# Performance work log

Hardware: AMD Instinct MI355X
Metric: run time of the kernel (lower is better)

## Reference

```python
import jax, jax.numpy as jnp
import numpy as np

NUM_HEADS = 16
ROPE_BASE = 10000.0


def _rope_cos_sin(seq_len, head_dim, dtype):
    # freqs for the half-dim; original caches cat(freqs, freqs) and then applies
    # the rotation per-half, which is equivalent to using the half-size tables.
    inv_freq = 1.0 / (ROPE_BASE ** (jnp.arange(0, head_dim, 2, dtype=jnp.float32) / head_dim))
    t = jnp.arange(seq_len, dtype=jnp.float32)
    freqs = jnp.einsum('i,j->ij', t, inv_freq)  # [S, hd/2]
    return jnp.cos(freqs).astype(dtype), jnp.sin(freqs).astype(dtype)


def _apply_rotary(x, cos, sin):
    # x: [B, H, S, hd]; cos/sin: [S, hd/2] broadcast over B, H
    half = x.shape[-1] // 2
    x1, x2 = x[..., :half], x[..., half:]
    return jnp.concatenate([x1 * cos - x2 * sin, x2 * cos + x1 * sin], axis=-1)


def setup_inputs() -> dict:
    key = jax.random.key(0)
    ks = jax.random.split(key, 5)
    D = 2048
    B, S = 2, 2048
    std = 1.0 / np.sqrt(D)
    return {
        'x': jax.random.normal(ks[0], (B, S, D), dtype=jnp.float32),
        'Wq': jax.random.normal(ks[1], (D, D), dtype=jnp.float32) * std,
        'Wk': jax.random.normal(ks[2], (D, D), dtype=jnp.float32) * std,
        'Wv': jax.random.normal(ks[3], (D, D), dtype=jnp.float32) * std,
        'Wo': jax.random.normal(ks[4], (D, D), dtype=jnp.float32) * std,
    }


def reference(x, Wq, Wk, Wv, Wo):
    B, S, D = x.shape
    H = NUM_HEADS
    hd = D // H
    scale = hd ** -0.5

    def proj(W):  # torch Linear: y = x @ W.T -> [B, H, S, hd]
        return (x @ W.T).reshape(B, S, H, hd).transpose(0, 2, 1, 3)

    q, k, v = proj(Wq), proj(Wk), proj(Wv)

    cos, sin = _rope_cos_sin(S, hd, x.dtype)
    q = _apply_rotary(q, cos, sin)
    k = _apply_rotary(k, cos, sin)

    scores = jnp.einsum('bhqd,bhkd->bhqk', q, k) * scale  # full O(S^2) scores
    attn = jax.nn.softmax(scores, axis=-1)
    out = jnp.einsum('bhqk,bhkd->bhqd', attn, v)
    out = out.transpose(0, 2, 1, 3).reshape(B, S, D)
    return out @ Wo.T
```

## Files before the change

kernel.cpp:

```cpp
#include <hip/hip_runtime.h>
#include <cstdint>

typedef __attribute__((ext_vector_type(8))) short bf16x8;
typedef __attribute__((ext_vector_type(4))) float f32x4;
typedef __attribute__((ext_vector_type(16))) float f32x16;

__device__ inline unsigned short f2bf(float f) {
  uint32_t u = __float_as_uint(f);
  uint32_t lsb = (u >> 16) & 1u;
  u += 0x7fffu + lsb;
  return (unsigned short)(u >> 16);
}
__device__ inline float bf2f(unsigned short b) {
  return __uint_as_float(((uint32_t)b) << 16);
}
__device__ inline uint32_t cvt_pk_bf16(float lo, float hi) {
  uint32_t r;
  asm volatile("v_cvt_pk_bf16_f32 %0, %1, %2" : "=v"(r) : "v"(lo), "v"(hi));
  return r;
}

#define GLOAD16(gp, lp)                                                        \
  __builtin_amdgcn_global_load_lds(                                            \
      (const __attribute__((address_space(1))) void*)(gp),                     \
      (__attribute__((address_space(3))) void*)(lp), 16, 0, 0)

__global__ void cvt_f32_bf16(const float* __restrict__ in,
                             unsigned short* __restrict__ out, int n) {
  int i = (blockIdx.x * 256 + threadIdx.x) * 4;
  if (i >= n) return;
  float4 v = *(const float4*)(in + i);
  unsigned short o[4] = {f2bf(v.x), f2bf(v.y), f2bf(v.z), f2bf(v.w)};
  *(uint64_t*)(out + i) = *(const uint64_t*)o;
}

__global__ void rope_table_k(float* __restrict__ ctab, float* __restrict__ stab) {
  int i = blockIdx.x * 256 + threadIdx.x;
  int s = i >> 6, j = i & 63;
  float invf = expf(-(float)j * (9.210340371976184f / 64.0f));
  float ang = (float)s * invf;
  ctab[i] = cosf(ang);
  stab[i] = sinf(ang);
}

__global__ void rope_apply_k(unsigned short* __restrict__ qb,
                             unsigned short* __restrict__ kb,
                             const float* __restrict__ ctab,
                             const float* __restrict__ stab) {
  int row = blockIdx.x * 4 + (threadIdx.x >> 6);
  int t = threadIdx.x & 63;
  int s = row & 2047;
  int bh = (row >> 11) & 31;
  int isK = row >> 16;
  unsigned short* base = isK ? kb : qb;
  float qs = isK ? 1.0f : (0.08838834764831845f * 1.4426950408889634f);
  unsigned short* p = base + ((size_t)bh * 2048 + s) * 128;
  float c = ctab[s * 64 + t], sn = stab[s * 64 + t];
  float x1 = bf2f(p[t]), x2 = bf2f(p[t + 64]);
  p[t] = f2bf((x1 * c - x2 * sn) * qs);
  p[t + 64] = f2bf((x2 * c + x1 * sn) * qs);
}

__global__ void transpose_v_k(const unsigned short* __restrict__ v,
                              unsigned short* __restrict__ vt) {
  __shared__ unsigned short tile[64][72];
  int bh = blockIdx.x, st = blockIdx.y, dt = blockIdx.z;
  const unsigned short* src = v + ((size_t)bh * 2048 + st * 64) * 128 + dt * 64;
  unsigned short* dst = vt + ((size_t)bh * 128 + dt * 64) * 2048 + st * 64;
  int t = threadIdx.x;
  int r = t >> 2, c0 = (t & 3) * 16;
  *(bf16x8*)&tile[r][c0] = *(const bf16x8*)(src + (size_t)r * 128 + c0);
  *(bf16x8*)&tile[r][c0 + 8] = *(const bf16x8*)(src + (size_t)r * 128 + c0 + 8);
  __syncthreads();
  unsigned short o[16];
#pragma unroll
  for (int i = 0; i < 16; i++) o[i] = tile[c0 + i][r];
  *(bf16x8*)(dst + (size_t)r * 2048 + c0) = *(const bf16x8*)&o[0];
  *(bf16x8*)(dst + (size_t)r * 2048 + c0 + 8) = *(const bf16x8*)&o[8];
}

template <int EPI>
__global__ __launch_bounds__(256, 2) void gemm_bt(
    const unsigned short* __restrict__ A, const unsigned short* __restrict__ Bm,
    float* __restrict__ Cf, unsigned short* __restrict__ q_out,
    unsigned short* __restrict__ k_out, unsigned short* __restrict__ v_out,
    int M, int N, int K) {
  __shared__ unsigned short sA[128 * 32];
  __shared__ unsigned short sB[128 * 32];
  const int t = threadIdx.x;
  const int w = t >> 6, l = t & 63;
  const int wr = w >> 1, wc = w & 1;
  const int bm = blockIdx.x * 128, bn = blockIdx.y * 128;
  const int lr = l & 15, lg = l >> 4;
  f32x4 acc[4][4] = {};

  const int srow = w * 16 + (l >> 2);
  const int sseg = (l & 3) * 8;
  const unsigned short* ga = A + (size_t)(bm + srow) * K + sseg;
  const unsigned short* gb = Bm + (size_t)(bn + srow) * K + sseg;
  unsigned short* lA = sA + w * 512 + l * 8;
  unsigned short* lB = sB + w * 512 + l * 8;

  for (int kt = 0; kt < K; kt += 32) {
    __syncthreads();
    GLOAD16(ga + kt, lA);
    GLOAD16(ga + kt + (size_t)64 * K, lA + 2048);
    GLOAD16(gb + kt, lB);
    GLOAD16(gb + kt + (size_t)64 * K, lB + 2048);
    __syncthreads();
    bf16x8 af[4], bfv[4];
#pragma unroll
    for (int m = 0; m < 4; m++)
      af[m] = *(const bf16x8*)(sA + (wr * 64 + m * 16 + lr) * 32 + lg * 8);
#pragma unroll
    for (int n = 0; n < 4; n++)
      bfv[n] = *(const bf16x8*)(sB + (wc * 64 + n * 16 + lr) * 32 + lg * 8);
#pragma unroll
    for (int m = 0; m < 4; m++)
#pragma unroll
      for (int n = 0; n < 4; n++)
        acc[m][n] = __builtin_amdgcn_mfma_f32_16x16x32_bf16(af[m], bfv[n],
                                                            acc[m][n], 0, 0, 0);
  }

#pragma unroll
  for (int m = 0; m < 4; m++) {
#pragma unroll
    for (int n = 0; n < 4; n++) {
      int gm0 = bm + wr * 64 + m * 16 + lg * 4;
      int gn = bn + wc * 64 + n * 16 + lr;
#pragma unroll
      for (int j = 0; j < 4; j++) {
        float v = acc[m][n][j];
        int gm = gm0 + j;
        if (EPI == 0) {
          Cf[(size_t)gm * N + gn] = v;
        } else {
          int which = gn >> 11, rem = gn & 2047;
          int h = rem >> 7, d = rem & 127;
          int b = gm >> 11, s = gm & 2047;
          unsigned short* dst = which == 0 ? q_out : (which == 1 ? k_out : v_out);
          dst[(((size_t)(b * 16 + h)) * 2048 + s) * 128 + d] = f2bf(v);
        }
      }
    }
  }
}

__global__ __launch_bounds__(256, 2) void attn_k(
    const unsigned short* __restrict__ Q, const unsigned short* __restrict__ K,
    const unsigned short* __restrict__ Vt, unsigned short* __restrict__ ctx) {
  __shared__ unsigned short sK[2][64 * 128];
  __shared__ unsigned short sV[2][128 * 64];

  const int qt = blockIdx.x, bh = blockIdx.y;
  const int t = threadIdx.x;
  const int w = t >> 6, l = t & 63;
  const int lq = l & 31;
  const int h5 = l >> 5;
  const int b = bh >> 4, hh = bh & 15;
  const int q0 = qt * 128 + w * 32;
  const unsigned short* Qp = Q + ((size_t)bh * 2048 + q0) * 128;
  const unsigned short* Kbh = K + (size_t)bh * 2048 * 128;
  const unsigned short* Vbh = Vt + (size_t)bh * 128 * 2048;

  int gko[4], gvo[4];
#pragma unroll
  for (int i = 0; i < 4; i++) {
    int p = i * 256 + t;
    int rK = p >> 4, cK = p & 15;
    gko[i] = rK * 128 + ((cK ^ (rK & 7)) * 8);
    int rV = p >> 3, cV = p & 7;
    gvo[i] = rV * 2048 + ((cV ^ (rV & 7)) * 8);
  }

  bf16x8 qf[8];
#pragma unroll
  for (int st = 0; st < 8; st++)
    qf[st] = *(const bf16x8*)(Qp + lq * 128 + st * 16 + h5 * 8);

  f32x16 o[4];
#pragma unroll
  for (int db = 0; db < 4; db++) o[db] = (f32x16)0.0f;
  float m_r = -1e30f, l_r = 0.0f;

#define STAGE_KV(buf, kv)                                                      \
  do {                                                                         \
    _Pragma("unroll") for (int i = 0; i < 4; i++)                              \
        GLOAD16(Kbh + (size_t)(kv)*128 + gko[i],                               \
                sK[buf] + (i * 256 + t) * 8);                                  \
    _Pragma("unroll") for (int i = 0; i < 4; i++)                              \
        GLOAD16(Vbh + (size_t)(kv) + gvo[i], sV[buf] + (i * 256 + t) * 8);     \
  } while (0)

  STAGE_KV(0, 0);
  __syncthreads();

  for (int it = 0; it < 32; ++it) {
    const int cur = it & 1;
    if (it < 31) STAGE_KV(cur ^ 1, (it + 1) * 64);

    const char* kbuf = (const char*)sK[cur];
    const char* vbuf = (const char*)sV[cur];

    f32x16 s2[2];
#pragma unroll
    for (int kb2 = 0; kb2 < 2; kb2++) {
      s2[kb2] = (f32x16)0.0f;
      const int rr = kb2 * 32 + lq;
      const int swz = (rr & 7) << 4;
#pragma unroll
      for (int st = 0; st < 8; st++) {
        bf16x8 kf = *(const bf16x8*)(kbuf + rr * 256 + ((st * 32 + h5 * 16) ^ swz));
        s2[kb2] = __builtin_amdgcn_mfma_f32_32x32x16_bf16(kf, qf[st], s2[kb2], 0, 0, 0);
      }
    }

    float sm[32];
#pragma unroll
    for (int kb2 = 0; kb2 < 2; kb2++)
#pragma unroll
      for (int r = 0; r < 16; r++) sm[kb2 * 16 + r] = s2[kb2][r];

    float tmax = sm[0];
#pragma unroll
    for (int i = 1; i < 32; i++) tmax = fmaxf(tmax, sm[i]);
    tmax = fmaxf(tmax, __shfl_xor(tmax, 32));

    if (!__all(tmax <= m_r + 8.0f)) {
      float m_new = fmaxf(m_r, tmax);
      float fac = exp2f(m_r - m_new);
      l_r *= fac;
      float fo[16];
#pragma unroll
      for (int r = 0; r < 16; r++)
        fo[r] = __shfl(fac, (r & 3) + 8 * (r >> 2) + 4 * h5);
#pragma unroll
      for (int db = 0; db < 4; db++)
#pragma unroll
        for (int r = 0; r < 16; r++) o[db][r] *= fo[r];
      m_r = m_new;
    }

    float psum = 0.0f;
#pragma unroll
    for (int i = 0; i < 32; i++) {
      sm[i] = exp2f(sm[i] - m_r);
      psum += sm[i];
    }
    psum += __shfl_xor(psum, 32);
    l_r += psum;

    uint32_t wAp[2][4], wBp[2][4];
#pragma unroll
    for (int kb2 = 0; kb2 < 2; kb2++)
#pragma unroll
      for (int rq = 0; rq < 4; rq++) {
        wAp[kb2][rq] = cvt_pk_bf16(sm[kb2 * 16 + rq * 4 + 0], sm[kb2 * 16 + rq * 4 + 1]);
        wBp[kb2][rq] = cvt_pk_bf16(sm[kb2 * 16 + rq * 4 + 2], sm[kb2 * 16 + rq * 4 + 3]);
      }

#pragma unroll
    for (int st = 0; st < 4; st++) {
      const int kb2 = st >> 1, p2 = (st & 1) * 2;
      uint32_t keepA = h5 ? wAp[kb2][p2 + 1] : wAp[kb2][p2];
      uint32_t keepB = h5 ? wBp[kb2][p2 + 1] : wBp[kb2][p2];
      uint32_t sendA = h5 ? wAp[kb2][p2] : wAp[kb2][p2 + 1];
      uint32_t sendB = h5 ? wBp[kb2][p2] : wBp[kb2][p2 + 1];
      uint32_t partA = __shfl_xor(sendA, 32);
      uint32_t partB = __shfl_xor(sendB, 32);
      union {
        uint32_t u[4];
        bf16x8 v;
      } pu;
      pu.u[0] = h5 ? partA : keepA;
      pu.u[1] = h5 ? partB : keepB;
      pu.u[2] = h5 ? keepA : partA;
      pu.u[3] = h5 ? keepB : partB;
#pragma unroll
      for (int db = 0; db < 4; db++) {
        const int rv = db * 32 + lq;
        const int swz = (rv & 7) << 4;
        bf16x8 vb = *(const bf16x8*)(vbuf + rv * 128 + ((st * 32 + h5 * 16) ^ swz));
        o[db] = __builtin_amdgcn_mfma_f32_32x32x16_bf16(pu.v, vb, o[db], 0, 0, 0);
      }
    }
    __syncthreads();
  }

  float inv = 1.0f / l_r;
  float io[16];
#pragma unroll
  for (int r = 0; r < 16; r++)
    io[r] = __shfl(inv, (r & 3) + 8 * (r >> 2) + 4 * h5);
#pragma unroll
  for (int db = 0; db < 4; db++) {
#pragma unroll
    for (int r = 0; r < 16; r++) {
      int s = q0 + (r & 3) + 8 * (r >> 2) + 4 * h5;
      ctx[((size_t)(b * 2048 + s)) * 2048 + hh * 128 + db * 32 + lq] =
          f2bf(o[db][r] * io[r]);
    }
  }
}

extern "C" void kernel_launch(void* const* d_in, const int* in_sizes, int n_in,
                              void* d_out, int out_size, void* d_ws,
                              size_t ws_size, hipStream_t stream) {
  const float* x = (const float*)d_in[0];
  const float* Wq = (const float*)d_in[1];
  const float* Wk = (const float*)d_in[2];
  const float* Wv = (const float*)d_in[3];
  const float* Wo = (const float*)d_in[4];
  float* out = (float*)d_out;

  const size_t BS = 4096;
  const size_t D = 2048;

  char* p = (char*)d_ws;
  unsigned short* xb = (unsigned short*)p;   p += BS * D * 2;
  unsigned short* wqkv = (unsigned short*)p; p += 3 * D * D * 2;
  unsigned short* wo = (unsigned short*)p;   p += D * D * 2;
  unsigned short* qb = (unsigned short*)p;   p += BS * D * 2;
  unsigned short* kb = (unsigned short*)p;   p += BS * D * 2;
  unsigned short* vb = (unsigned short*)p;   p += BS * D * 2;
  float* ctab = (float*)p;                   p += 2048 * 64 * 4;
  float* stab = (float*)p;                   p += 2048 * 64 * 4;
  unsigned short* vt = wqkv;
  unsigned short* ctx = xb;

  cvt_f32_bf16<<<8388608 / 1024, 256, 0, stream>>>(x, xb, 8388608);
  cvt_f32_bf16<<<4194304 / 1024, 256, 0, stream>>>(Wq, wqkv, 4194304);
  cvt_f32_bf16<<<4194304 / 1024, 256, 0, stream>>>(Wk, wqkv + 4194304, 4194304);
  cvt_f32_bf16<<<4194304 / 1024, 256, 0, stream>>>(Wv, wqkv + 8388608, 4194304);
  cvt_f32_bf16<<<4194304 / 1024, 256, 0, stream>>>(Wo, wo, 4194304);
  rope_table_k<<<131072 / 256, 256, 0, stream>>>(ctab, stab);

  gemm_bt<1><<<dim3(32, 48), 256, 0, stream>>>(xb, wqkv, nullptr, qb, kb, vb,
                                               4096, 6144, 2048);
  rope_apply_k<<<32768, 256, 0, stream>>>(qb, kb, ctab, stab);
  transpose_v_k<<<dim3(32, 32, 2), 256, 0, stream>>>(vb, vt);
  attn_k<<<dim3(16, 32), 256, 0, stream>>>(qb, kb, vt, ctx);
  gemm_bt<0><<<dim3(32, 16), 256, 0, stream>>>(ctx, wo, out, nullptr, nullptr,
                                               nullptr, 4096, 2048, 2048);
}
```

Baseline: 316.3 us.

## Add 256x256-tile 8-wave GEMM with XCD swizzle for QKV projection

Introduces a new GEMM kernel with 256x256 output tiles, 512 threads, and a double-buffered, K-split LDS pipeline. It interleaves global-to-LDS loads with MFMA phases, using explicit barriers, waitcnts and setprio. Blocks are remapped so that neighbouring tiles land on the same XCD for L2 reuse. The QKV projection now uses this kernel, aiming for more data reuse per tile and better overlap of loads with compute. In exchange it runs one block per CU with high register use, and the hand-written waitcnt and barrier choreography is fragile.

```diff
diff --git a/kernel.cpp b/kernel.cpp
--- a/kernel.cpp
+++ b/kernel.cpp
@@ -147,6 +147,159 @@
   }
 }
 
+template <int EPI>
+__global__ __launch_bounds__(512, 1) void gemm256(
+    const unsigned short* __restrict__ A, const unsigned short* __restrict__ Bm,
+    float* __restrict__ Cf, unsigned short* __restrict__ q_out,
+    unsigned short* __restrict__ k_out, unsigned short* __restrict__ v_out,
+    int M, int N, int K, int nbm) {
+  __shared__ unsigned short sA[2][2][256 * 32];
+  __shared__ unsigned short sB[2][2][256 * 32];
+
+  const int t = threadIdx.x;
+  const int w = t >> 6, l = t & 63;
+  const int wr = w >> 2, wc = w & 3;
+  const int lr = l & 15, lg = l >> 4;
+  const int gsw = (lg ^ (lr & 3)) * 8;
+
+  const int cpx = gridDim.x >> 3;
+  const int bid = blockIdx.x;
+  const int swz = (bid & 7) * cpx + (bid >> 3);
+  const int bm = (swz % nbm) * 256, bn = (swz / nbm) * 256;
+
+  f32x4 acc[8][4] = {};
+
+  int rowi[2], goff[2];
+#pragma unroll
+  for (int i = 0; i < 2; i++) {
+    int idx = i * 512 + t;
+    rowi[i] = idx >> 2;
+    goff[i] = ((idx & 3) ^ (rowi[i] & 3)) * 8;
+  }
+  const unsigned short* Ab = A + (size_t)bm * K;
+  const unsigned short* Bb = Bm + (size_t)bn * K;
+
+#define STAGE256(Xb, plane, koff)                                              \
+  do {                                                                         \
+    _Pragma("unroll") for (int i = 0; i < 2; i++)                              \
+        GLOAD16(Xb + (size_t)rowi[i] * K + (koff) + goff[i],                   \
+                (plane) + (i * 512 + t) * 8);                                  \
+  } while (0)
+
+  STAGE256(Ab, sA[0][0], 0);
+  STAGE256(Bb, sB[0][0], 0);
+  STAGE256(Ab, sA[0][1], 32);
+  STAGE256(Bb, sB[0][1], 32);
+  asm volatile("s_waitcnt vmcnt(4)" ::: "memory");
+  __builtin_amdgcn_s_barrier();
+
+  const int NT = K >> 6;
+  for (int t2 = 0; t2 < NT; ++t2) {
+    const int db = t2 & 1, dn = db ^ 1;
+    const int kt = (t2 + 1 < NT ? t2 + 1 : t2) * 64;
+    bf16x8 a[4], a2[4], b[4];
+
+#pragma unroll
+    for (int mf = 0; mf < 4; mf++)
+      a[mf] = *(const bf16x8*)&sA[db][0][(wr * 128 + mf * 16 + lr) * 32 + gsw];
+#pragma unroll
+    for (int nf = 0; nf < 4; nf++)
+      b[nf] = *(const bf16x8*)&sB[db][0][(wc * 64 + nf * 16 + lr) * 32 + gsw];
+    STAGE256(Ab, sA[dn][0], kt);
+    __builtin_amdgcn_s_barrier();
+    asm volatile("s_waitcnt lgkmcnt(0)" ::: "memory");
+    __builtin_amdgcn_sched_barrier(0);
+    __builtin_amdgcn_s_setprio(1);
+#pragma unroll
+    for (int mf = 0; mf < 4; mf++)
+#pragma unroll
+      for (int nf = 0; nf < 4; nf++)
+        acc[mf][nf] = __builtin_amdgcn_mfma_f32_16x16x32_bf16(a[mf], b[nf],
+                                                              acc[mf][nf], 0, 0, 0);
+    __builtin_amdgcn_s_setprio(0);
+    __builtin_amdgcn_s_barrier();
+
+#pragma unroll
+    for (int mf = 0; mf < 4; mf++)
+      a2[mf] = *(const bf16x8*)&sA[db][0][(wr * 128 + (mf + 4) * 16 + lr) * 32 + gsw];
+    STAGE256(Bb, sB[dn][0], kt);
+    __builtin_amdgcn_s_barrier();
+    asm volatile("s_waitcnt lgkmcnt(0)" ::: "memory");
+    __builtin_amdgcn_sched_barrier(0);
+    __builtin_amdgcn_s_setprio(1);
+#pragma unroll
+    for (int mf = 0; mf < 4; mf++)
+#pragma unroll
+      for (int nf = 0; nf < 4; nf++)
+        acc[mf + 4][nf] = __builtin_amdgcn_mfma_f32_16x16x32_bf16(
+            a2[mf], b[nf], acc[mf + 4][nf], 0, 0, 0);
+    __builtin_amdgcn_s_setprio(0);
+    asm volatile("s_waitcnt vmcnt(4)" ::: "memory");
+    __builtin_amdgcn_s_barrier();
+
+#pragma unroll
+    for (int mf = 0; mf < 4; mf++)
+      a[mf] = *(const bf16x8*)&sA[db][1][(wr * 128 + mf * 16 + lr) * 32 + gsw];
+#pragma unroll
+    for (int nf = 0; nf < 4; nf++)
+      b[nf] = *(const bf16x8*)&sB[db][1][(wc * 64 + nf * 16 + lr) * 32 + gsw];
+    STAGE256(Ab, sA[dn][1], kt + 32);
+    __builtin_amdgcn_s_barrier();
+    asm volatile("s_waitcnt lgkmcnt(0)" ::: "memory");
+    __builtin_amdgcn_sched_barrier(0);
+    __builtin_amdgcn_s_setprio(1);
+#pragma unroll
+    for (int mf = 0; mf < 4; mf++)
+#pragma unroll
+      for (int nf = 0; nf < 4; nf++)
+        acc[mf][nf] = __builtin_amdgcn_mfma_f32_16x16x32_bf16(a[mf], b[nf],
+                                                              acc[mf][nf], 0, 0, 0);
+    __builtin_amdgcn_s_setprio(0);
+    __builtin_amdgcn_s_barrier();
+
+#pragma unroll
+    for (int mf = 0; mf < 4; mf++)
+      a2[mf] = *(const bf16x8*)&sA[db][1][(wr * 128 + (mf + 4) * 16 + lr) * 32 + gsw];
+    STAGE256(Bb, sB[dn][1], kt + 32);
+    __builtin_amdgcn_s_barrier();
+    asm volatile("s_waitcnt lgkmcnt(0)" ::: "memory");
+    __builtin_amdgcn_sched_barrier(0);
+    __builtin_amdgcn_s_setprio(1);
+#pragma unroll
+    for (int mf = 0; mf < 4; mf++)
+#pragma unroll
+      for (int nf = 0; nf < 4; nf++)
+        acc[mf + 4][nf] = __builtin_amdgcn_mfma_f32_16x16x32_bf16(
+            a2[mf], b[nf], acc[mf + 4][nf], 0, 0, 0);
+    __builtin_amdgcn_s_setprio(0);
+    asm volatile("s_waitcnt vmcnt(4)" ::: "memory");
+    __builtin_amdgcn_s_barrier();
+  }
+
+#pragma unroll
+  for (int mf = 0; mf < 8; mf++) {
+#pragma unroll
+    for (int nf = 0; nf < 4; nf++) {
+      int gm0 = bm + wr * 128 + mf * 16 + lg * 4;
+      int gn = bn + wc * 64 + nf * 16 + lr;
+#pragma unroll
+      for (int j = 0; j < 4; j++) {
+        float v = acc[mf][nf][j];
+        int gm = gm0 + j;
+        if (EPI == 0) {
+          Cf[(size_t)gm * N + gn] = v;
+        } else {
+          int which = gn >> 11, rem = gn & 2047;
+          int h = rem >> 7, d = rem & 127;
+          int b = gm >> 11, s = gm & 2047;
+          unsigned short* dst = which == 0 ? q_out : (which == 1 ? k_out : v_out);
+          dst[(((size_t)(b * 16 + h)) * 2048 + s) * 128 + d] = f2bf(v);
+        }
+      }
+    }
+  }
+}
+
 __global__ __launch_bounds__(256, 2) void attn_k(
     const unsigned short* __restrict__ Q, const unsigned short* __restrict__ K,
     const unsigned short* __restrict__ Vt, unsigned short* __restrict__ ctx) {
@@ -208,10 +361,10 @@
     for (int kb2 = 0; kb2 < 2; kb2++) {
       s2[kb2] = (f32x16)0.0f;
       const int rr = kb2 * 32 + lq;
-      const int swz = (rr & 7) << 4;
+      const int swzz = (rr & 7) << 4;
 #pragma unroll
       for (int st = 0; st < 8; st++) {
-        bf16x8 kf = *(const bf16x8*)(kbuf + rr * 256 + ((st * 32 + h5 * 16) ^ swz));
+        bf16x8 kf = *(const bf16x8*)(kbuf + rr * 256 + ((st * 32 + h5 * 16) ^ swzz));
         s2[kb2] = __builtin_amdgcn_mfma_f32_32x32x16_bf16(kf, qf[st], s2[kb2], 0, 0, 0);
       }
     }
@@ -280,8 +433,8 @@
 #pragma unroll
       for (int db = 0; db < 4; db++) {
         const int rv = db * 32 + lq;
-        const int swz = (rv & 7) << 4;
-        bf16x8 vb = *(const bf16x8*)(vbuf + rv * 128 + ((st * 32 + h5 * 16) ^ swz));
+        const int swzz = (rv & 7) << 4;
+        bf16x8 vb = *(const bf16x8*)(vbuf + rv * 128 + ((st * 32 + h5 * 16) ^ swzz));
         o[db] = __builtin_amdgcn_mfma_f32_32x32x16_bf16(pu.v, vb, o[db], 0, 0, 0);
       }
     }
@@ -336,8 +489,8 @@
   cvt_f32_bf16<<<4194304 / 1024, 256, 0, stream>>>(Wo, wo, 4194304);
   rope_table_k<<<131072 / 256, 256, 0, stream>>>(ctab, stab);
 
-  gemm_bt<1><<<dim3(32, 48), 256, 0, stream>>>(xb, wqkv, nullptr, qb, kb, vb,
-                                               4096, 6144, 2048);
+  gemm256<1><<<384, 512, 0, stream>>>(xb, wqkv, nullptr, qb, kb, vb, 4096, 6144,
+                                      2048, 16);
   rope_apply_k<<<32768, 256, 0, stream>>>(qb, kb, ctab, stab);
   transpose_v_k<<<dim3(32, 32, 2), 256, 0, stream>>>(vb, vt);
   attn_k<<<dim3(16, 32), 256, 0, stream>>>(qb, kb, vt, ctx);
```

Result: slower. 355.6 us (+12.4%).
